# Optimization experiments

Hardware: AMD Instinct MI355X
Metric: run time of the kernel (lower is better)

The kernel has to match this reference:

```python
import jax, jax.numpy as jnp
import numpy as np
from jax import lax

B, T, D, H = 128, 129, 128, 64  # batch, window, input_size (num driving series), hidden_size
Tm1 = T - 1


def setup_inputs() -> dict:
    key = jax.random.key(0)
    ks = jax.random.split(key, 11)
    s = 0.05
    return {
        "input_data": jax.random.normal(ks[0], (B, Tm1, D), jnp.float32),
        "W_ehs_w": jax.random.normal(ks[1], (Tm1, 2 * H), jnp.float32) * s,
        "W_ehs_b": jax.random.normal(ks[2], (Tm1,), jnp.float32) * s,
        "U_e_w": jax.random.normal(ks[3], (Tm1, Tm1), jnp.float32) * s,
        "U_e_b": jax.random.normal(ks[4], (Tm1,), jnp.float32) * s,
        "v_e_w": jax.random.normal(ks[5], (1, Tm1), jnp.float32) * s,
        "v_e_b": jax.random.normal(ks[6], (1,), jnp.float32) * s,
        "W_ih": jax.random.normal(ks[7], (4 * H, D), jnp.float32) * s,
        "W_hh": jax.random.normal(ks[8], (4 * H, H), jnp.float32) * s,
        "b_ih": jax.random.normal(ks[9], (4 * H,), jnp.float32) * s,
        "b_hh": jax.random.normal(ks[10], (4 * H,), jnp.float32) * s,
    }


def reference(input_data, W_ehs_w, W_ehs_b, U_e_w, U_e_b, v_e_w, v_e_b, W_ih, W_hh, b_ih, b_hh):
    # input_data: [B, T-1, D]
    dt = input_data.dtype
    # U_e applied to each driving series' full history; constant across t.
    # x_k = input.permute(0,2,1) -> [B, D, T-1]; Linear: x @ W.T + b
    x_perm = jnp.transpose(input_data, (0, 2, 1))            # [B, D, T-1]
    Ue_x = jnp.einsum("bdt,st->bds", x_perm, U_e_w) + U_e_b  # [B, D, T-1]

    def step(carry, x_t):
        h, c = carry                                          # each [B, H]
        # In the torch code (h,c) are broadcast identically over the D axis,
        # so compute W_ehs once per batch row and broadcast.
        hc = jnp.concatenate([h, c], axis=-1)                 # [B, 2H]
        we = hc @ W_ehs_w.T + W_ehs_b                         # [B, T-1]
        z = jnp.tanh(we[:, None, :] + Ue_x)                   # [B, D, T-1]
        v = z @ v_e_w[0] + v_e_b[0]                           # [B, D]
        a = jax.nn.softmax(v, axis=1)                         # softmax over drivers
        x_hat = a * x_t                                       # [B, D]
        # single LSTM step (torch gate order: i, f, g, o)
        gates = x_hat @ W_ih.T + b_ih + h @ W_hh.T + b_hh     # [B, 4H]
        i, f, g, o = jnp.split(gates, 4, axis=1)
        c_new = jax.nn.sigmoid(f) * c + jax.nn.sigmoid(i) * jnp.tanh(g)
        h_new = jax.nn.sigmoid(o) * jnp.tanh(c_new)
        return (h_new, c_new), (x_hat, h_new)

    h0 = jnp.zeros((input_data.shape[0], H), dt)
    c0 = jnp.zeros((input_data.shape[0], H), dt)
    xs = jnp.transpose(input_data, (1, 0, 2))                 # time-major [T-1, B, D]
    _, (xw, he) = lax.scan(step, (h0, c0), xs)
    input_weighted = jnp.transpose(xw, (1, 0, 2))             # [B, T-1, D]
    input_encoded = jnp.transpose(he, (1, 0, 2))              # [B, T-1, H]
    return input_weighted, input_encoded
```

## Files before the change

### kernel.cpp

```cpp
#include <hip/hip_runtime.h>
#include <hip/hip_bf16.h>
#include <hip/hip_fp16.h>

#define NB 128
#define NT 128
#define ND 128
#define NH 64
#define NTH 1024
#define ESTR 144

typedef float f32x2 __attribute__((ext_vector_type(2)));
typedef _Float16 f16x2 __attribute__((ext_vector_type(2)));

__device__ __forceinline__ float fexp2(float x) { return __builtin_amdgcn_exp2f(x); }
__device__ __forceinline__ float frcp (float x) { return __builtin_amdgcn_rcpf(x); }

template<int CTRL>
__device__ __forceinline__ float dppadd(float v) {
  return v + __int_as_float(__builtin_amdgcn_update_dpp(
      0, __float_as_int(v), CTRL, 0xF, 0xF, true));
}
__device__ __forceinline__ float sum16(float v) {
  v = dppadd<0xB1>(v);
  v = dppadd<0x4E>(v);
  v = dppadd<0x141>(v);
  v = dppadd<0x140>(v);
  return v;
}

__device__ __forceinline__ unsigned short f2bf(float f) {
  unsigned u = __float_as_uint(f);
  u += 0x7fffu + ((u >> 16) & 1u);
  return (unsigned short)(u >> 16);
}
__device__ __forceinline__ float blo(unsigned u) { return __uint_as_float(u << 16); }
__device__ __forceinline__ float bhi(unsigned u) { return __uint_as_float(u & 0xffff0000u); }

__device__ __forceinline__ __half2 uh(unsigned u) {
  union { unsigned u; __half2 h; } x; x.u = u; return x.h;
}
__device__ __forceinline__ unsigned hu(__half2 h) {
  union { unsigned u; __half2 h; } x; x.h = h; return x.u;
}
__device__ __forceinline__ f16x2 uh2(unsigned u) {
  union { unsigned u; f16x2 h; } x; x.u = u; return x.h;
}
__device__ __forceinline__ unsigned pkf16(float lo, float hi) {
  return hu(__halves2half2(__float2half_rn(lo), __float2half_rn(hi)));
}

__device__ __forceinline__ float dot2(unsigned a, unsigned b, float c) {
#if __has_builtin(__builtin_amdgcn_fdot2)
  return __builtin_amdgcn_fdot2(uh2(a), uh2(b), c, false);
#else
  const __half2 p = __hmul2(uh(a), uh(b));
  return c + __low2float(p) + __high2float(p);
#endif
}

#define PIN(v) asm volatile("" : "+v"(v))

__global__ __launch_bounds__(NTH)
__attribute__((amdgpu_waves_per_eu(4, 4)))
void darnn_enc(
    const float* __restrict__ x,
    const float* __restrict__ Wehs,
    const float* __restrict__ behs,
    const float* __restrict__ Ue,
    const float* __restrict__ Ueb,
    const float* __restrict__ vew,
    const float* __restrict__ Wih,
    const float* __restrict__ Whh,
    const float* __restrict__ bih,
    const float* __restrict__ bhh,
    float* __restrict__ out)
{
  constexpr float C2  = 2.88539008177792681f;
  constexpr float L2E = 1.44269504088896340f;

  __shared__ __align__(16) float          xh[NT][ND];
  __shared__ __align__(16) unsigned short Ebt[ND][ESTR];
  __shared__ __align__(16) float          hbuf[NT][NH];
  __shared__ __align__(16) unsigned       hcpk[2][8][12];
  __shared__ __align__(16) float          cq[2][16][6];
  __shared__ __align__(16) float          wvm[16][12];
  __shared__ __align__(16) unsigned       xpk[16][12];
  __shared__ __align__(16) float          part64[64];
  __shared__ __align__(16) float          rsb[NT];

  const int b    = blockIdx.x;
  const int tid  = threadIdx.x;
  const int lane = tid & 63;
  const int wid  = tid >> 6;
  const float* xb = x + b * (NT * ND);

#pragma unroll
  for (int i = 0; i < 4; ++i) {
    const int f = i * 1024 + tid;
    const int t = f >> 5, c = (f & 31) << 2;
    *reinterpret_cast<float4*>(&xh[t][c]) =
        *reinterpret_cast<const float4*>(xb + t * ND + c);
  }
  float (*UeTc)[33] = reinterpret_cast<float(*)[33]>(&hbuf[0][0]);
  __syncthreads();

  {
    const int dq = tid & 31;
    const int sg = tid >> 5;
    float acc[16];
#pragma unroll
    for (int i = 0; i < 16; ++i) acc[i] = 0.f;
    for (int c = 0; c < 4; ++c) {
      {
        const int ss = 32 * c + sg;
        const int t4 = dq * 4;
        const float4 u4 = *reinterpret_cast<const float4*>(Ue + ss * NT + t4);
        UeTc[t4 + 0][sg] = u4.x;
        UeTc[t4 + 1][sg] = u4.y;
        UeTc[t4 + 2][sg] = u4.z;
        UeTc[t4 + 3][sg] = u4.w;
      }
      __syncthreads();
#pragma unroll 4
      for (int t = 0; t < NT; ++t) {
        const float4 xv = *reinterpret_cast<const float4*>(&xh[t][4 * dq]);
        const float u = UeTc[t][sg];
        acc[4*c+0] = fmaf(xv.x, u, acc[4*c+0]);
        acc[4*c+1] = fmaf(xv.y, u, acc[4*c+1]);
        acc[4*c+2] = fmaf(xv.z, u, acc[4*c+2]);
        acc[4*c+3] = fmaf(xv.w, u, acc[4*c+3]);
      }
      __syncthreads();
    }
#pragma unroll
    for (int c = 0; c < 4; ++c) {
      const int ss = sg + 32 * c;
      const float ub = Ueb[ss];
#pragma unroll
      for (int di = 0; di < 4; ++di) {
        const float e = fexp2(C2 * (acc[4*c+di] + ub));
        Ebt[4*dq + di][ss] = f2bf(e);
      }
    }
  }
  __syncthreads();

  if (tid < 192) (&hcpk[0][0][0])[tid] = 0u;
  if (tid < 192) (&cq[0][0][0])[tid] = 0.f;

  const int s_a = tid >> 3, r_a = tid & 7;
  unsigned wehs_p[8];
#pragma unroll
  for (int i = 0; i < 4; ++i) {
    const float4 v4 = *reinterpret_cast<const float4*>(Wehs + s_a * 128 + r_a * 16 + 4 * i);
    wehs_p[2*i]   = pkf16(v4.x, v4.y);
    wehs_p[2*i+1] = pkf16(v4.z, v4.w);
  }
  float behs_r = behs[s_a];

  const int s_l = lane & 15;
  const int dp  = lane >> 4;
  const int d0  = 8 * wid + 2 * dp;
  f32x2 mv[4];
  {
    const float4 va = *reinterpret_cast<const float4*>(vew + 8 * s_l);
    const float4 vb = *reinterpret_cast<const float4*>(vew + 8 * s_l + 4);
    mv[0] = (f32x2){-2.f * va.x, -2.f * va.y};
    mv[1] = (f32x2){-2.f * va.z, -2.f * va.w};
    mv[2] = (f32x2){-2.f * vb.x, -2.f * vb.y};
    mv[3] = (f32x2){-2.f * vb.z, -2.f * vb.w};
  }
  f32x2 er2[8];
  {
    const int4 ea = *reinterpret_cast<const int4*>(&Ebt[d0][8 * s_l]);
    const int4 eb = *reinterpret_cast<const int4*>(&Ebt[d0 + 1][8 * s_l]);
    er2[0] = (f32x2){blo((unsigned)ea.x), bhi((unsigned)ea.x)};
    er2[1] = (f32x2){blo((unsigned)ea.y), bhi((unsigned)ea.y)};
    er2[2] = (f32x2){blo((unsigned)ea.z), bhi((unsigned)ea.z)};
    er2[3] = (f32x2){blo((unsigned)ea.w), bhi((unsigned)ea.w)};
    er2[4] = (f32x2){blo((unsigned)eb.x), bhi((unsigned)eb.x)};
    er2[5] = (f32x2){blo((unsigned)eb.y), bhi((unsigned)eb.y)};
    er2[6] = (f32x2){blo((unsigned)eb.z), bhi((unsigned)eb.z)};
    er2[7] = (f32x2){blo((unsigned)eb.w), bhi((unsigned)eb.w)};
  }

  const int kk = lane >> 4, cD = lane & 15;
  const int kD = 4 * wid + kk;
  unsigned wx2[16], wh2[8];
  float b4[4];
#pragma unroll
  for (int g = 0; g < 4; ++g) {
    const int j = 64 * g + kD;
    const float4 u0 = *reinterpret_cast<const float4*>(Wih + j * 128 + 8 * cD);
    const float4 u1 = *reinterpret_cast<const float4*>(Wih + j * 128 + 8 * cD + 4);
    wx2[4*g]   = pkf16(u0.x, u0.y);
    wx2[4*g+1] = pkf16(u0.z, u0.w);
    wx2[4*g+2] = pkf16(u1.x, u1.y);
    wx2[4*g+3] = pkf16(u1.z, u1.w);
    const float4 u2 = *reinterpret_cast<const float4*>(Whh + j * 64 + 4 * cD);
    wh2[2*g]   = pkf16(u2.x, u2.y);
    wh2[2*g+1] = pkf16(u2.z, u2.w);
    b4[g] = bih[j] + bhh[j];
  }

#pragma unroll
  for (int i = 0; i < 8; ++i) PIN(wehs_p[i]);
#pragma unroll
  for (int i = 0; i < 8; ++i) PIN(er2[i]);
#pragma unroll
  for (int i = 0; i < 4; ++i) PIN(mv[i]);
#pragma unroll
  for (int i = 0; i < 16; ++i) PIN(wx2[i]);
#pragma unroll
  for (int i = 0; i < 8; ++i) PIN(wh2[i]);
#pragma unroll
  for (int g = 0; g < 4; ++g) PIN(b4[g]);
  PIN(behs_r);

  __syncthreads();

  int p = 0;
  for (int t = 0; t < NT; ++t) {
    const float2 xv = *reinterpret_cast<const float2*>(&xh[t][d0]);

    {
      const int4 q0 = *reinterpret_cast<const int4*>(&hcpk[p][r_a][0]);
      const int4 q1 = *reinterpret_cast<const int4*>(&hcpk[p][r_a][4]);
      float a0 = 0.f, a1 = 0.f;
      a0 = dot2((unsigned)q0.x, wehs_p[0], a0);
      a1 = dot2((unsigned)q0.y, wehs_p[1], a1);
      a0 = dot2((unsigned)q0.z, wehs_p[2], a0);
      a1 = dot2((unsigned)q0.w, wehs_p[3], a1);
      a0 = dot2((unsigned)q1.x, wehs_p[4], a0);
      a1 = dot2((unsigned)q1.y, wehs_p[5], a1);
      a0 = dot2((unsigned)q1.z, wehs_p[6], a0);
      a1 = dot2((unsigned)q1.w, wehs_p[7], a1);
      float a = a0 + a1;
      a = dppadd<0xB1>(a);
      a = dppadd<0x4E>(a);
      a = dppadd<0x141>(a);
      if (r_a == 0) wvm[s_a >> 3][s_a & 7] = fexp2(C2 * (a + behs_r));
    }
    __syncthreads();

    int2 hh; float c_old;
    {
      const float4 wa = *reinterpret_cast<const float4*>(&wvm[s_l][0]);
      const float4 wb = *reinterpret_cast<const float4*>(&wvm[s_l][4]);
      hh    = *reinterpret_cast<const int2*>(&hcpk[p][cD >> 2][2 * (cD & 3)]);
      c_old = cq[p][wid][kk];
      const f32x2 one2 = {1.f, 1.f};
      const f32x2 w01 = {wa.x, wa.y}, w23 = {wa.z, wa.w};
      const f32x2 w45 = {wb.x, wb.y}, w67 = {wb.z, wb.w};
      f32x2 ac0 = {0.f, 0.f}, ac0b = {0.f, 0.f};
      f32x2 ac1 = {0.f, 0.f}, ac1b = {0.f, 0.f};
#define BSTEP(W, E, M, ACC) do {                                   \
        f32x2 q_ = __builtin_elementwise_fma(W, E, one2);          \
        f32x2 r_; r_.x = frcp(q_.x); r_.y = frcp(q_.y);            \
        ACC = __builtin_elementwise_fma(M, r_, ACC);               \
      } while (0)
      BSTEP(w01, er2[0], mv[0], ac0);
      BSTEP(w23, er2[1], mv[1], ac0b);
      BSTEP(w45, er2[2], mv[2], ac0);
      BSTEP(w67, er2[3], mv[3], ac0b);
      BSTEP(w01, er2[4], mv[0], ac1);
      BSTEP(w23, er2[5], mv[1], ac1b);
      BSTEP(w45, er2[6], mv[2], ac1);
      BSTEP(w67, er2[7], mv[3], ac1b);
#undef BSTEP
      const f32x2 sv0 = ac0 + ac0b;
      const f32x2 sv1 = ac1 + ac1b;
      float s0 = sum16(sv0.x + sv0.y);
      float s1 = sum16(sv1.x + sv1.y);
      const float e0 = fexp2(L2E * s0);
      const float e1 = fexp2(L2E * s1);
      if (s_l == 0) {
        part64[4 * wid + dp] = e0 + e1;
        xpk[wid][dp] = pkf16(e0 * xv.x, e1 * xv.y);
        *reinterpret_cast<float2*>(&xh[t][d0]) =
            make_float2(e0 * xv.x, e1 * xv.y);
      }
    }
    __syncthreads();

    {
      float tot = part64[lane];
      tot = sum16(tot);
      tot += __int_as_float(__builtin_amdgcn_ds_swizzle(__float_as_int(tot), 0x401F));
      tot += __shfl_xor(tot, 32);
      const float rs = frcp(tot);
      const int4 xq = *reinterpret_cast<const int4*>(&xpk[cD][0]);
      const __half2 rsh = __half2half2(__float2half_rn(rs));
      const unsigned xs0 = hu(__hmul2(uh((unsigned)xq.x), rsh));
      const unsigned xs1 = hu(__hmul2(uh((unsigned)xq.y), rsh));
      const unsigned xs2 = hu(__hmul2(uh((unsigned)xq.z), rsh));
      const unsigned xs3 = hu(__hmul2(uh((unsigned)xq.w), rsh));
      float ac[4];
#pragma unroll
      for (int g = 0; g < 4; ++g) {
        float s = 0.f;
        s = dot2(xs0, wx2[4*g],   s);
        s = dot2(xs1, wx2[4*g+1], s);
        s = dot2(xs2, wx2[4*g+2], s);
        s = dot2(xs3, wx2[4*g+3], s);
        s = dot2((unsigned)hh.x, wh2[2*g],   s);
        s = dot2((unsigned)hh.y, wh2[2*g+1], s);
        ac[g] = sum16(s);
      }
      const float gi = ac[0] + b4[0];
      const float gf = ac[1] + b4[1];
      const float gG = ac[2] + b4[2];
      const float go = ac[3] + b4[3];
      const float si = frcp(1.f + fexp2(-L2E * gi));
      const float sf = frcp(1.f + fexp2(-L2E * gf));
      const float tg = 1.f - 2.f * frcp(1.f + fexp2(C2 * gG));
      const float cn = fmaf(sf, c_old, si * tg);
      const float so = frcp(1.f + fexp2(-L2E * go));
      const float tc = 1.f - 2.f * frcp(1.f + fexp2(C2 * cn));
      const float hn = so * tc;
      if (cD == 0) {
        __half* Hb = reinterpret_cast<__half*>(&hcpk[p ^ 1][0][0]);
        Hb[(kD >> 4) * 24 + (kD & 15)]       = __float2half_rn(hn);
        Hb[(4 + (kD >> 4)) * 24 + (kD & 15)] = __float2half_rn(cn);
        cq[p ^ 1][wid][kk] = cn;
        hbuf[t][kD] = hn;
      }
      if (tid == 0) rsb[t] = rs;
    }
    __syncthreads();
    p ^= 1;
  }

#pragma unroll
  for (int i = 0; i < 4; ++i) {
    const int f = i * 1024 + tid;
    const int t = f >> 5, c = (f & 31) << 2;
    float4 v = *reinterpret_cast<const float4*>(&xh[t][c]);
    const float rs = rsb[t];
    v.x *= rs; v.y *= rs; v.z *= rs; v.w *= rs;
    *reinterpret_cast<float4*>(out + b * (NT * ND) + t * ND + c) = v;
  }
  float* out2 = out + NB * (NT * ND) + b * (NT * NH);
#pragma unroll
  for (int i = 0; i < 2; ++i) {
    const int f = i * 1024 + tid;
    const int t = f >> 4, c = (f & 15) << 2;
    *reinterpret_cast<float4*>(out2 + t * NH + c) =
        *reinterpret_cast<const float4*>(&hbuf[t][c]);
  }
}

extern "C" void kernel_launch(void* const* d_in, const int* in_sizes, int n_in,
                              void* d_out, int out_size, void* d_ws, size_t ws_size,
                              hipStream_t stream) {
  const float* x    = (const float*)d_in[0];
  const float* Wehs = (const float*)d_in[1];
  const float* behs = (const float*)d_in[2];
  const float* Ue   = (const float*)d_in[3];
  const float* Ueb  = (const float*)d_in[4];
  const float* vew  = (const float*)d_in[5];
  const float* Wih  = (const float*)d_in[7];
  const float* Whh  = (const float*)d_in[8];
  const float* bih  = (const float*)d_in[9];
  const float* bhh  = (const float*)d_in[10];
  float* out = (float*)d_out;

  darnn_enc<<<NB, NTH, 0, stream>>>(x, Wehs, behs, Ue, Ueb, vew, Wih, Whh, bih, bhh, out);
}
```

Before: 270.8 us.

## Fold exp2 scale constants into weights, defer softmax normalization, unroll timestep loop by two

Pre-scales the W_ehs weights and bias by C2 and v_e by -2*log2(e), which removes per-step multiplies before exp2. The x-side gate dot products are now computed on the unnormalized attention-weighted inputs, in parallel with the softmax-sum reduction. The reciprocal is then applied with one fma per gate, replacing the packed half multiplies that sat on the critical path. The time loop is unrolled by two with constant buffer parity, removing the dynamic ping-pong index. The unnormalized f16 values may have larger magnitude, which risks precision loss or overflow.

```diff
diff --git a/kernel.cpp b/kernel.cpp
--- a/kernel.cpp
+++ b/kernel.cpp
@@ -153,10 +153,10 @@
 #pragma unroll
   for (int i = 0; i < 4; ++i) {
     const float4 v4 = *reinterpret_cast<const float4*>(Wehs + s_a * 128 + r_a * 16 + 4 * i);
-    wehs_p[2*i]   = pkf16(v4.x, v4.y);
-    wehs_p[2*i+1] = pkf16(v4.z, v4.w);
-  }
-  float behs_r = behs[s_a];
+    wehs_p[2*i]   = pkf16(C2 * v4.x, C2 * v4.y);
+    wehs_p[2*i+1] = pkf16(C2 * v4.z, C2 * v4.w);
+  }
+  float behs_r = C2 * behs[s_a];
 
   const int s_l = lane & 15;
   const int dp  = lane >> 4;
@@ -165,10 +165,11 @@
   {
     const float4 va = *reinterpret_cast<const float4*>(vew + 8 * s_l);
     const float4 vb = *reinterpret_cast<const float4*>(vew + 8 * s_l + 4);
-    mv[0] = (f32x2){-2.f * va.x, -2.f * va.y};
-    mv[1] = (f32x2){-2.f * va.z, -2.f * va.w};
-    mv[2] = (f32x2){-2.f * vb.x, -2.f * vb.y};
-    mv[3] = (f32x2){-2.f * vb.z, -2.f * vb.w};
+    const float k = -2.f * L2E;
+    mv[0] = (f32x2){k * va.x, k * va.y};
+    mv[1] = (f32x2){k * va.z, k * va.w};
+    mv[2] = (f32x2){k * vb.x, k * vb.y};
+    mv[3] = (f32x2){k * vb.z, k * vb.w};
   }
   f32x2 er2[8];
   {
@@ -219,117 +220,119 @@
 
   __syncthreads();
 
-  int p = 0;
-  for (int t = 0; t < NT; ++t) {
-    const float2 xv = *reinterpret_cast<const float2*>(&xh[t][d0]);
-
-    {
-      const int4 q0 = *reinterpret_cast<const int4*>(&hcpk[p][r_a][0]);
-      const int4 q1 = *reinterpret_cast<const int4*>(&hcpk[p][r_a][4]);
-      float a0 = 0.f, a1 = 0.f;
-      a0 = dot2((unsigned)q0.x, wehs_p[0], a0);
-      a1 = dot2((unsigned)q0.y, wehs_p[1], a1);
-      a0 = dot2((unsigned)q0.z, wehs_p[2], a0);
-      a1 = dot2((unsigned)q0.w, wehs_p[3], a1);
-      a0 = dot2((unsigned)q1.x, wehs_p[4], a0);
-      a1 = dot2((unsigned)q1.y, wehs_p[5], a1);
-      a0 = dot2((unsigned)q1.z, wehs_p[6], a0);
-      a1 = dot2((unsigned)q1.w, wehs_p[7], a1);
-      float a = a0 + a1;
-      a = dppadd<0xB1>(a);
-      a = dppadd<0x4E>(a);
-      a = dppadd<0x141>(a);
-      if (r_a == 0) wvm[s_a >> 3][s_a & 7] = fexp2(C2 * (a + behs_r));
-    }
-    __syncthreads();
-
-    int2 hh; float c_old;
-    {
-      const float4 wa = *reinterpret_cast<const float4*>(&wvm[s_l][0]);
-      const float4 wb = *reinterpret_cast<const float4*>(&wvm[s_l][4]);
-      hh    = *reinterpret_cast<const int2*>(&hcpk[p][cD >> 2][2 * (cD & 3)]);
-      c_old = cq[p][wid][kk];
-      const f32x2 one2 = {1.f, 1.f};
-      const f32x2 w01 = {wa.x, wa.y}, w23 = {wa.z, wa.w};
-      const f32x2 w45 = {wb.x, wb.y}, w67 = {wb.z, wb.w};
-      f32x2 ac0 = {0.f, 0.f}, ac0b = {0.f, 0.f};
-      f32x2 ac1 = {0.f, 0.f}, ac1b = {0.f, 0.f};
+#define STEP(T, P) do {                                                        \
+    const float2 xv = *reinterpret_cast<const float2*>(&xh[(T)][d0]);          \
+     {                          \
+      const int4 q0 = *reinterpret_cast<const int4*>(&hcpk[(P)][r_a][0]);      \
+      const int4 q1 = *reinterpret_cast<const int4*>(&hcpk[(P)][r_a][4]);      \
+      float a0 = 0.f, a1 = 0.f;                                                \
+      a0 = dot2((unsigned)q0.x, wehs_p[0], a0);                                \
+      a1 = dot2((unsigned)q0.y, wehs_p[1], a1);                                \
+      a0 = dot2((unsigned)q0.z, wehs_p[2], a0);                                \
+      a1 = dot2((unsigned)q0.w, wehs_p[3], a1);                                \
+      a0 = dot2((unsigned)q1.x, wehs_p[4], a0);                                \
+      a1 = dot2((unsigned)q1.y, wehs_p[5], a1);                                \
+      a0 = dot2((unsigned)q1.z, wehs_p[6], a0);                                \
+      a1 = dot2((unsigned)q1.w, wehs_p[7], a1);                                \
+      float a = a0 + a1;                                                       \
+      a = dppadd<0xB1>(a);                                                     \
+      a = dppadd<0x4E>(a);                                                     \
+      a = dppadd<0x141>(a);                                                    \
+      if (r_a == 0) wvm[s_a >> 3][s_a & 7] = fexp2(a + behs_r);                \
+    }                                                                          \
+    __syncthreads();                                                           \
+    int2 hh; float c_old;                                                      \
+     {                      \
+      const float4 wa = *reinterpret_cast<const float4*>(&wvm[s_l][0]);        \
+      const float4 wb = *reinterpret_cast<const float4*>(&wvm[s_l][4]);        \
+      hh    = *reinterpret_cast<const int2*>(&hcpk[(P)][cD >> 2][2 * (cD & 3)]); \
+      c_old = cq[(P)][wid][kk];                                                \
+      const f32x2 one2 = {1.f, 1.f};                                           \
+      const f32x2 w01 = {wa.x, wa.y}, w23 = {wa.z, wa.w};                      \
+      const f32x2 w45 = {wb.x, wb.y}, w67 = {wb.z, wb.w};                      \
+      f32x2 ac0 = {0.f, 0.f}, ac0b = {0.f, 0.f};                               \
+      f32x2 ac1 = {0.f, 0.f}, ac1b = {0.f, 0.f};                               \
+      BSTEP(w01, er2[0], mv[0], ac0);                                          \
+      BSTEP(w23, er2[1], mv[1], ac0b);                                         \
+      BSTEP(w45, er2[2], mv[2], ac0);                                          \
+      BSTEP(w67, er2[3], mv[3], ac0b);                                         \
+      BSTEP(w01, er2[4], mv[0], ac1);                                          \
+      BSTEP(w23, er2[5], mv[1], ac1b);                                         \
+      BSTEP(w45, er2[6], mv[2], ac1);                                          \
+      BSTEP(w67, er2[7], mv[3], ac1b);                                         \
+      const f32x2 sv0 = ac0 + ac0b;                                            \
+      const f32x2 sv1 = ac1 + ac1b;                                            \
+      float s0 = sum16(sv0.x + sv0.y);                                         \
+      float s1 = sum16(sv1.x + sv1.y);                                         \
+      const float e0 = fexp2(s0);                                              \
+      const float e1 = fexp2(s1);                                              \
+      if (s_l == 0) {                                                          \
+        part64[4 * wid + dp] = e0 + e1;                                        \
+        xpk[wid][dp] = pkf16(e0 * xv.x, e1 * xv.y);                            \
+        *reinterpret_cast<float2*>(&xh[(T)][d0]) =                             \
+            make_float2(e0 * xv.x, e1 * xv.y);                                 \
+      }                                                                        \
+    }                                                                          \
+    __syncthreads();                                                           \
+     {     \
+      const int4 xq = *reinterpret_cast<const int4*>(&xpk[cD][0]);             \
+      float sx[4], sh[4];                                                      \
+      _Pragma("unroll")                                                        \
+      for (int g = 0; g < 4; ++g) {                                            \
+        float s = 0.f;                                                         \
+        s = dot2((unsigned)xq.x, wx2[4*g],   s);                               \
+        s = dot2((unsigned)xq.y, wx2[4*g+1], s);                               \
+        s = dot2((unsigned)xq.z, wx2[4*g+2], s);                               \
+        s = dot2((unsigned)xq.w, wx2[4*g+3], s);                               \
+        sx[g] = s;                                                             \
+        float h = 0.f;                                                         \
+        h = dot2((unsigned)hh.x, wh2[2*g],   h);                               \
+        h = dot2((unsigned)hh.y, wh2[2*g+1], h);                               \
+        sh[g] = h;                                                             \
+      }                                                                        \
+      float tot = part64[lane];                                                \
+      tot = sum16(tot);                                                        \
+      tot += __int_as_float(__builtin_amdgcn_ds_swizzle(__float_as_int(tot), 0x401F)); \
+      tot += __shfl_xor(tot, 32);                                              \
+      const float rs = frcp(tot);                                              \
+      float ac[4];                                                             \
+      _Pragma("unroll")                                                        \
+      for (int g = 0; g < 4; ++g) ac[g] = sum16(fmaf(sx[g], rs, sh[g]));       \
+      const float gi = ac[0] + b4[0];                                          \
+      const float gf = ac[1] + b4[1];                                          \
+      const float gG = ac[2] + b4[2];                                          \
+      const float go = ac[3] + b4[3];                                          \
+      const float si = frcp(1.f + fexp2(-L2E * gi));                           \
+      const float sf = frcp(1.f + fexp2(-L2E * gf));                           \
+      const float tg = 1.f - 2.f * frcp(1.f + fexp2(C2 * gG));                 \
+      const float cn = fmaf(sf, c_old, si * tg);                               \
+      const float so = frcp(1.f + fexp2(-L2E * go));                           \
+      const float tc = 1.f - 2.f * frcp(1.f + fexp2(C2 * cn));                 \
+      const float hn = so * tc;                                                \
+      if (cD == 0) {                                                           \
+        __half* Hb = reinterpret_cast<__half*>(&hcpk[(P) ^ 1][0][0]);          \
+        Hb[(kD >> 4) * 24 + (kD & 15)]       = __float2half_rn(hn);            \
+        Hb[(4 + (kD >> 4)) * 24 + (kD & 15)] = __float2half_rn(cn);            \
+        cq[(P) ^ 1][wid][kk] = cn;                                             \
+        hbuf[(T)][kD] = hn;                                                    \
+      }                                                                        \
+      if (tid == 0) rsb[(T)] = rs;                                             \
+    }                                                                          \
+    __syncthreads();                                                           \
+  } while (0)
+
 #define BSTEP(W, E, M, ACC) do {                                   \
-        f32x2 q_ = __builtin_elementwise_fma(W, E, one2);          \
-        f32x2 r_; r_.x = frcp(q_.x); r_.y = frcp(q_.y);            \
-        ACC = __builtin_elementwise_fma(M, r_, ACC);               \
-      } while (0)
-      BSTEP(w01, er2[0], mv[0], ac0);
-      BSTEP(w23, er2[1], mv[1], ac0b);
-      BSTEP(w45, er2[2], mv[2], ac0);
-      BSTEP(w67, er2[3], mv[3], ac0b);
-      BSTEP(w01, er2[4], mv[0], ac1);
-      BSTEP(w23, er2[5], mv[1], ac1b);
-      BSTEP(w45, er2[6], mv[2], ac1);
-      BSTEP(w67, er2[7], mv[3], ac1b);
+    f32x2 q_ = __builtin_elementwise_fma(W, E, one2);              \
+    f32x2 r_; r_.x = frcp(q_.x); r_.y = frcp(q_.y);                \
+    ACC = __builtin_elementwise_fma(M, r_, ACC);                   \
+  } while (0)
+
+  for (int t = 0; t < NT; t += 2) {
+    STEP(t, 0);
+    STEP(t + 1, 1);
+  }
 #undef BSTEP
-      const f32x2 sv0 = ac0 + ac0b;
-      const f32x2 sv1 = ac1 + ac1b;
-      float s0 = sum16(sv0.x + sv0.y);
-      float s1 = sum16(sv1.x + sv1.y);
-      const float e0 = fexp2(L2E * s0);
-      const float e1 = fexp2(L2E * s1);
-      if (s_l == 0) {
-        part64[4 * wid + dp] = e0 + e1;
-        xpk[wid][dp] = pkf16(e0 * xv.x, e1 * xv.y);
-        *reinterpret_cast<float2*>(&xh[t][d0]) =
-            make_float2(e0 * xv.x, e1 * xv.y);
-      }
-    }
-    __syncthreads();
-
-    {
-      float tot = part64[lane];
-      tot = sum16(tot);
-      tot += __int_as_float(__builtin_amdgcn_ds_swizzle(__float_as_int(tot), 0x401F));
-      tot += __shfl_xor(tot, 32);
-      const float rs = frcp(tot);
-      const int4 xq = *reinterpret_cast<const int4*>(&xpk[cD][0]);
-      const __half2 rsh = __half2half2(__float2half_rn(rs));
-      const unsigned xs0 = hu(__hmul2(uh((unsigned)xq.x), rsh));
-      const unsigned xs1 = hu(__hmul2(uh((unsigned)xq.y), rsh));
-      const unsigned xs2 = hu(__hmul2(uh((unsigned)xq.z), rsh));
-      const unsigned xs3 = hu(__hmul2(uh((unsigned)xq.w), rsh));
-      float ac[4];
-#pragma unroll
-      for (int g = 0; g < 4; ++g) {
-        float s = 0.f;
-        s = dot2(xs0, wx2[4*g],   s);
-        s = dot2(xs1, wx2[4*g+1], s);
-        s = dot2(xs2, wx2[4*g+2], s);
-        s = dot2(xs3, wx2[4*g+3], s);
-        s = dot2((unsigned)hh.x, wh2[2*g],   s);
-        s = dot2((unsigned)hh.y, wh2[2*g+1], s);
-        ac[g] = sum16(s);
-      }
-      const float gi = ac[0] + b4[0];
-      const float gf = ac[1] + b4[1];
-      const float gG = ac[2] + b4[2];
-      const float go = ac[3] + b4[3];
-      const float si = frcp(1.f + fexp2(-L2E * gi));
-      const float sf = frcp(1.f + fexp2(-L2E * gf));
-      const float tg = 1.f - 2.f * frcp(1.f + fexp2(C2 * gG));
-      const float cn = fmaf(sf, c_old, si * tg);
-      const float so = frcp(1.f + fexp2(-L2E * go));
-      const float tc = 1.f - 2.f * frcp(1.f + fexp2(C2 * cn));
-      const float hn = so * tc;
-      if (cD == 0) {
-        __half* Hb = reinterpret_cast<__half*>(&hcpk[p ^ 1][0][0]);
-        Hb[(kD >> 4) * 24 + (kD & 15)]       = __float2half_rn(hn);
-        Hb[(4 + (kD >> 4)) * 24 + (kD & 15)] = __float2half_rn(cn);
-        cq[p ^ 1][wid][kk] = cn;
-        hbuf[t][kD] = hn;
-      }
-      if (tid == 0) rsb[t] = rs;
-    }
-    __syncthreads();
-    p ^= 1;
-  }
+#undef STEP
 
 #pragma unroll
   for (int i = 0; i < 4; ++i) {
```

Result: faster. 265.0 us (-2.1%).
